# Performance work log

Measured on AMD Instinct MI355X. Metric: run time of the kernel, lower is better.

Reference implementation:

```python
import jax, jax.numpy as jnp
import numpy as np
from jax.ops import segment_sum, segment_max

N = 10000       # nodes
E = 320000      # edges (avg degree 32)
IN_FEATS = 256
HID = 128
HEADS = 4


def setup_inputs() -> dict:
    key = jax.random.key(0)
    ks = jax.random.split(key, 12)
    s = lambda fan_in: 1.0 / np.sqrt(fan_in)
    return {
        "features": jax.random.normal(ks[0], (N, IN_FEATS), jnp.float32),
        "src": jax.random.randint(ks[1], (E,), 0, N, jnp.int32),
        "dst": jax.random.randint(ks[2], (E,), 0, N, jnp.int32),
        # GraphConv 1: in_feats -> hidden
        "W1": jax.random.normal(ks[3], (IN_FEATS, HID), jnp.float32) * s(IN_FEATS),
        "b1": jnp.zeros((HID,), jnp.float32),
        # GraphConv 2: hidden -> hidden
        "W2": jax.random.normal(ks[4], (HID, HID), jnp.float32) * s(HID),
        "b2": jnp.zeros((HID,), jnp.float32),
        # GraphConv 3: hidden -> 1
        "W3": jax.random.normal(ks[5], (HID, 1), jnp.float32) * s(HID),
        "b3": jnp.zeros((1,), jnp.float32),
        # GATConv(hidden, hidden, num_heads=4)
        "Wg": jax.random.normal(ks[6], (HID, HEADS * HID), jnp.float32) * s(HID),
        "attn_l": jax.random.normal(ks[7], (HEADS, HID), jnp.float32) * s(HID),
        "attn_r": jax.random.normal(ks[8], (HEADS, HID), jnp.float32) * s(HID),
        "bg": jnp.zeros((HEADS * HID,), jnp.float32),
    }


def _graph_conv(src, dst, x, W, b):
    """DGL GraphConv with norm='both': D_dst^{-1/2} A D_src^{-1/2} x W + b."""
    ones = jnp.ones((src.shape[0],), x.dtype)
    deg_out = jnp.clip(segment_sum(ones, src, num_segments=N), 1.0)
    deg_in = jnp.clip(segment_sum(ones, dst, num_segments=N), 1.0)
    h = (x * deg_out[:, None] ** -0.5) @ W          # [N, out]
    agg = segment_sum(h[src], dst, num_segments=N)   # gather+scatter over edges
    return agg * deg_in[:, None] ** -0.5 + b


def _gat_conv(src, dst, x, Wg, attn_l, attn_r, bg):
    """DGL GATConv, num_heads=4, negative_slope=0.2. Returns (out, alpha)."""
    z = (x @ Wg).reshape(N, HEADS, HID)             # [N,H,D]
    el = jnp.einsum("nhd,hd->nh", z, attn_l)        # [N,H]
    er = jnp.einsum("nhd,hd->nh", z, attn_r)
    e = jax.nn.leaky_relu(el[src] + er[dst], 0.2)   # [E,H]
    # edge softmax over incoming edges of each dst node
    m = segment_max(e, dst, num_segments=N)          # [N,H]
    ex = jnp.exp(e - m[dst])
    denom = segment_sum(ex, dst, num_segments=N)     # [N,H]
    alpha = ex / denom[dst]                          # [E,H]
    out = segment_sum(alpha[:, :, None] * z[src], dst, num_segments=N)  # [N,H,D]
    return out + bg.reshape(1, HEADS, HID), alpha


def reference(features, src, dst, W1, b1, W2, b2, W3, b3, Wg, attn_l, attn_r, bg):
    h = jax.nn.relu(_graph_conv(src, dst, features, W1, b1))
    h = jax.nn.relu(_graph_conv(src, dst, h, W2, b2))
    h, alpha = _gat_conv(src, dst, h, Wg, attn_l, attn_r, bg)
    h = h.mean(axis=1)                               # mean over heads -> [N,HID]
    risk_scores = jax.nn.sigmoid(_graph_conv(src, dst, h, W3, b3))  # [N,1]
    return risk_scores
```

## Files before the change

kernel.cpp:

```cpp
#include <hip/hip_runtime.h>
#include <hip/hip_bf16.h>

#define NODES   10000
#define EDGES   320000
#define INF_    256
#define HIDF    128
#define NHEADS  4
#define SLOTS   64

#define NB_W1     128
#define NB_ZERO   79
#define PREP_BLKS (NB_W1 + NB_ZERO)

#define FILL_BLKS  1250
#define G1_TILES   157
#define B_W2T      (FILL_BLKS + G1_TILES)
#define NB_W2      64
#define B_FOLD     (B_W2T + NB_W2)
#define B_CDOT     (B_FOLD + 2)
#define FG_BLKS    (B_CDOT + 1)

typedef __attribute__((ext_vector_type(8))) short short8v;
typedef __attribute__((ext_vector_type(4))) float f32x4;

__device__ __forceinline__ float bf_lo(unsigned z) { return __uint_as_float(z << 16); }
__device__ __forceinline__ float bf_hi(unsigned z) { return __uint_as_float(z & 0xffff0000u); }
__device__ __forceinline__ unsigned short bfr(float x) {
    __hip_bfloat16 b = __float2bfloat16(x);
    return *(unsigned short*)&b;
}

__global__ __launch_bounds__(256)
void prep_slim(const float* __restrict__ W1, unsigned short* __restrict__ W1t,
               int* __restrict__ cnt_dego) {
    int b = blockIdx.x, t = threadIdx.x;
    if (b < NB_W1) {
        int id = b * 256 + t;
        int nn = id >> 8, k = id & 255;
        W1t[id] = bfr(W1[k * HIDF + nn]);
        return;
    }
    int id = (b - NB_W1) * 256 + t;
    if (id < 2 * NODES) cnt_dego[id] = 0;
}

__global__ __launch_bounds__(256)
void fill_gemm1(const int* __restrict__ src, const int* __restrict__ dst,
                int* __restrict__ cnt, int* __restrict__ deg_o,
                unsigned short* __restrict__ csr, const float* __restrict__ feat,
                const unsigned short* __restrict__ W1t, unsigned short* __restrict__ Z1,
                const float* __restrict__ W2, unsigned short* __restrict__ W2t,
                const float* __restrict__ Wg, const float* __restrict__ attn_l,
                const float* __restrict__ attn_r, const float* __restrict__ bg,
                const float* __restrict__ W3, float* __restrict__ WL,
                float* __restrict__ WR, float* __restrict__ WV, float* __restrict__ cdot) {
    int b = blockIdx.x, t = threadIdx.x;
    if (b < FILL_BLKS) {
        int e = b * 256 + t;
        int s = src[e], d = dst[e];
        atomicAdd(&deg_o[s], 1);
        int pos = atomicAdd(&cnt[d], 1);
        csr[(d << 6) + pos] = (unsigned short)s;
        return;
    }
    if (b < B_W2T) {
        int vt = b - FILL_BLKS;
        int w = t >> 6, l = t & 63;
        int m0 = vt * 64 + w * 16;
        int lm = l & 15, lk = (l >> 4) * 8;
        int arow = min(m0 + lm, NODES - 1);
        const float4* Af = (const float4*)(feat + (size_t)arow * INF_ + lk);
        const short8v* Bp[8];
#pragma unroll
        for (int cg = 0; cg < 8; ++cg)
            Bp[cg] = (const short8v*)(W1t + (size_t)(cg * 16 + lm) * INF_ + lk);
        f32x4 acc[8];
#pragma unroll
        for (int cg = 0; cg < 8; ++cg) acc[cg] = (f32x4){0.f, 0.f, 0.f, 0.f};
#pragma unroll
        for (int kk = 0; kk < 8; ++kk) {
            float4 f0 = Af[kk * 8];
            float4 f1 = Af[kk * 8 + 1];
            short8v a = {(short)bfr(f0.x), (short)bfr(f0.y), (short)bfr(f0.z), (short)bfr(f0.w),
                         (short)bfr(f1.x), (short)bfr(f1.y), (short)bfr(f1.z), (short)bfr(f1.w)};
#pragma unroll
            for (int cg = 0; cg < 8; ++cg)
                acc[cg] = __builtin_amdgcn_mfma_f32_16x16x32_bf16(a, Bp[cg][kk * 4], acc[cg], 0, 0, 0);
        }
        int rb = m0 + (l >> 4) * 4;
#pragma unroll
        for (int cg = 0; cg < 8; ++cg) {
            int c = cg * 16 + lm;
#pragma unroll
            for (int r = 0; r < 4; ++r) {
                int row = rb + r;
                if (row < NODES) Z1[(size_t)row * HIDF + c] = bfr(acc[cg][r]);
            }
        }
        return;
    }
    if (b < B_FOLD) {
        int id = (b - B_W2T) * 256 + t;
        int nn = id >> 7, k = id & 127;
        W2t[id] = bfr(W2[k * HIDF + nn]);
        return;
    }
    if (b < B_CDOT) {
        int id = (b - B_FOLD) * 256 + t;
        int k = id >> 2, h = id & 3;
        float a = 0.f, bb = 0.f, c = 0.f;
        for (int d = 0; d < HIDF; ++d) {
            float w = Wg[k * 512 + h * HIDF + d];
            a  = fmaf(w, attn_l[h * HIDF + d], a);
            bb = fmaf(w, attn_r[h * HIDF + d], bb);
            c  = fmaf(w, W3[d], c);
        }
        WL[id] = a; WR[id] = bb; WV[id] = c;
        return;
    }
    {
        if (t < 64) {
            float s = 0.f;
            for (int d = t; d < HIDF; d += 64)
                s += (bg[d] + bg[d + 128] + bg[d + 256] + bg[d + 384]) * W3[d];
#pragma unroll
            for (int off = 32; off; off >>= 1) s += __shfl_xor(s, off, 64);
            if (t == 0) cdot[0] = 0.25f * s;
        }
    }
}

__global__ __launch_bounds__(256)
void g1_gemm2(const int* __restrict__ deg_i, const int* __restrict__ deg_o,
              const unsigned short* __restrict__ csr, const unsigned short* __restrict__ Z1,
              const float* __restrict__ b1, const unsigned short* __restrict__ W2t,
              unsigned short* __restrict__ Z2) {
    __shared__ unsigned short Ht[16][136];
    int t = threadIdx.x;
    int w = t >> 6, l = t & 63;
    int m0 = blockIdx.x * 16;
    int quarter = l >> 4, q = l & 15;
    for (int j = 0; j < 4; ++j) {
        int nl = w * 4 + j;
        int n = m0 + nl;
        float a[8] = {0.f, 0.f, 0.f, 0.f, 0.f, 0.f, 0.f, 0.f};
        float sc = 0.f, so = 0.f;
        if (n < NODES) {
            int cnt = deg_i[n];
            int base = n << 6;
            int i = quarter;
            for (; i + 4 < cnt; i += 8) {
                int s0 = csr[base + i], s1 = csr[base + i + 4];
                float so0 = rsqrtf(fmaxf((float)deg_o[s0], 1.f));
                float so1 = rsqrtf(fmaxf((float)deg_o[s1], 1.f));
                uint4 z0 = *(const uint4*)&Z1[s0 * HIDF + 8 * q];
                uint4 z1 = *(const uint4*)&Z1[s1 * HIDF + 8 * q];
                a[0] = fmaf(so0, bf_lo(z0.x), a[0]); a[1] = fmaf(so0, bf_hi(z0.x), a[1]);
                a[2] = fmaf(so0, bf_lo(z0.y), a[2]); a[3] = fmaf(so0, bf_hi(z0.y), a[3]);
                a[4] = fmaf(so0, bf_lo(z0.z), a[4]); a[5] = fmaf(so0, bf_hi(z0.z), a[5]);
                a[6] = fmaf(so0, bf_lo(z0.w), a[6]); a[7] = fmaf(so0, bf_hi(z0.w), a[7]);
                a[0] = fmaf(so1, bf_lo(z1.x), a[0]); a[1] = fmaf(so1, bf_hi(z1.x), a[1]);
                a[2] = fmaf(so1, bf_lo(z1.y), a[2]); a[3] = fmaf(so1, bf_hi(z1.y), a[3]);
                a[4] = fmaf(so1, bf_lo(z1.z), a[4]); a[5] = fmaf(so1, bf_hi(z1.z), a[5]);
                a[6] = fmaf(so1, bf_lo(z1.w), a[6]); a[7] = fmaf(so1, bf_hi(z1.w), a[7]);
            }
            if (i < cnt) {
                int s0 = csr[base + i];
                float so0 = rsqrtf(fmaxf((float)deg_o[s0], 1.f));
                uint4 z0 = *(const uint4*)&Z1[s0 * HIDF + 8 * q];
                a[0] = fmaf(so0, bf_lo(z0.x), a[0]); a[1] = fmaf(so0, bf_hi(z0.x), a[1]);
                a[2] = fmaf(so0, bf_lo(z0.y), a[2]); a[3] = fmaf(so0, bf_hi(z0.y), a[3]);
                a[4] = fmaf(so0, bf_lo(z0.z), a[4]); a[5] = fmaf(so0, bf_hi(z0.z), a[5]);
                a[6] = fmaf(so0, bf_lo(z0.w), a[6]); a[7] = fmaf(so0, bf_hi(z0.w), a[7]);
            }
            sc = rsqrtf(fmaxf((float)cnt, 1.f));
            so = rsqrtf(fmaxf((float)deg_o[n], 1.f));
        }
#pragma unroll
        for (int k = 0; k < 8; ++k) {
            a[k] += __shfl_xor(a[k], 16, 64);
            a[k] += __shfl_xor(a[k], 32, 64);
        }
        if (l < 16) {
            float v[8];
#pragma unroll
            for (int k = 0; k < 8; ++k)
                v[k] = fmaxf(fmaf(a[k], sc, b1[8 * q + k]), 0.f) * so;
            uint4 o;
            o.x = ((unsigned)bfr(v[1]) << 16) | bfr(v[0]);
            o.y = ((unsigned)bfr(v[3]) << 16) | bfr(v[2]);
            o.z = ((unsigned)bfr(v[5]) << 16) | bfr(v[4]);
            o.w = ((unsigned)bfr(v[7]) << 16) | bfr(v[6]);
            *(uint4*)&Ht[nl][8 * q] = o;
        }
    }
    __syncthreads();
    int lm = l & 15, lk = (l >> 4) * 8;
    const unsigned short* arow = &Ht[lm][lk];
    const short8v* Bp0 = (const short8v*)(W2t + (size_t)(w * 16 + lm) * HIDF + lk);
    const short8v* Bp1 = (const short8v*)(W2t + (size_t)((w + 4) * 16 + lm) * HIDF + lk);
    f32x4 acc0 = {0.f, 0.f, 0.f, 0.f}, acc1 = acc0;
#pragma unroll
    for (int kk = 0; kk < 4; ++kk) {
        short8v av = *(const short8v*)(arow + kk * 32);
        acc0 = __builtin_amdgcn_mfma_f32_16x16x32_bf16(av, Bp0[kk * 4], acc0, 0, 0, 0);
        acc1 = __builtin_amdgcn_mfma_f32_16x16x32_bf16(av, Bp1[kk * 4], acc1, 0, 0, 0);
    }
    int rb = m0 + (l >> 4) * 4;
#pragma unroll
    for (int r = 0; r < 4; ++r) {
        int row = rb + r;
        if (row < NODES) {
            Z2[(size_t)row * HIDF + w * 16 + lm]       = bfr(acc0[r]);
            Z2[(size_t)row * HIDF + (w + 4) * 16 + lm] = bfr(acc1[r]);
        }
    }
}

__global__ __launch_bounds__(64)
void gather2(const int* __restrict__ deg_i, const unsigned short* __restrict__ csr,
             const unsigned short* __restrict__ Z2, const float* __restrict__ b2,
             const float* __restrict__ WL, const float* __restrict__ WR,
             const float* __restrict__ WV, float* __restrict__ el,
             float* __restrict__ er, float* __restrict__ zeta) {
    int n = blockIdx.x, l = threadIdx.x;
    int quarter = l >> 4, q = l & 15;
    int cnt = deg_i[n], base = n << 6;
    float a[8] = {0.f, 0.f, 0.f, 0.f, 0.f, 0.f, 0.f, 0.f};
    int i = quarter;
    for (; i + 4 < cnt; i += 8) {
        int s0 = csr[base + i], s1 = csr[base + i + 4];
        uint4 z0 = *(const uint4*)&Z2[s0 * HIDF + 8 * q];
        uint4 z1 = *(const uint4*)&Z2[s1 * HIDF + 8 * q];
        a[0] += bf_lo(z0.x); a[1] += bf_hi(z0.x);
        a[2] += bf_lo(z0.y); a[3] += bf_hi(z0.y);
        a[4] += bf_lo(z0.z); a[5] += bf_hi(z0.z);
        a[6] += bf_lo(z0.w); a[7] += bf_hi(z0.w);
        a[0] += bf_lo(z1.x); a[1] += bf_hi(z1.x);
        a[2] += bf_lo(z1.y); a[3] += bf_hi(z1.y);
        a[4] += bf_lo(z1.z); a[5] += bf_hi(z1.z);
        a[6] += bf_lo(z1.w); a[7] += bf_hi(z1.w);
    }
    if (i < cnt) {
        int s0 = csr[base + i];
        uint4 z0 = *(const uint4*)&Z2[s0 * HIDF + 8 * q];
        a[0] += bf_lo(z0.x); a[1] += bf_hi(z0.x);
        a[2] += bf_lo(z0.y); a[3] += bf_hi(z0.y);
        a[4] += bf_lo(z0.z); a[5] += bf_hi(z0.z);
        a[6] += bf_lo(z0.w); a[7] += bf_hi(z0.w);
    }
#pragma unroll
    for (int k = 0; k < 8; ++k) {
        a[k] += __shfl_xor(a[k], 16, 64);
        a[k] += __shfl_xor(a[k], 32, 64);
    }
    float sc = rsqrtf(fmaxf((float)cnt, 1.f));
    float v[8];
#pragma unroll
    for (int k = 0; k < 8; ++k) v[k] = fmaxf(fmaf(a[k], sc, b2[8 * q + k]), 0.f);
    float elh[NHEADS] = {0.f, 0.f, 0.f, 0.f};
    float erh[NHEADS] = {0.f, 0.f, 0.f, 0.f};
    float zth[NHEADS] = {0.f, 0.f, 0.f, 0.f};
#pragma unroll
    for (int k = 0; k < 8; ++k) {
        int kc = 8 * q + k;
#pragma unroll
        for (int h = 0; h < NHEADS; ++h) {
            elh[h] = fmaf(v[k], WL[kc * NHEADS + h], elh[h]);
            erh[h] = fmaf(v[k], WR[kc * NHEADS + h], erh[h]);
            zth[h] = fmaf(v[k], WV[kc * NHEADS + h], zth[h]);
        }
    }
#pragma unroll
    for (int h = 0; h < NHEADS; ++h) {
#pragma unroll
        for (int off = 1; off <= 8; off <<= 1) {
            elh[h] += __shfl_xor(elh[h], off, 64);
            erh[h] += __shfl_xor(erh[h], off, 64);
            zth[h] += __shfl_xor(zth[h], off, 64);
        }
    }
    if (l == 0) {
#pragma unroll
        for (int h = 0; h < NHEADS; ++h) {
            el[n * NHEADS + h] = elh[h];
            er[n * NHEADS + h] = erh[h];
            zeta[n * NHEADS + h] = zth[h];
        }
    }
}

__global__ __launch_bounds__(64)
void gat_s1(const int* __restrict__ deg_i, const int* __restrict__ deg_o,
            const unsigned short* __restrict__ csr, const float4* __restrict__ el4,
            const float4* __restrict__ er4, const float4* __restrict__ zeta4,
            const float* __restrict__ cdot, float* __restrict__ s1v) {
    int n = blockIdx.x, l = threadIdx.x;
    int cnt = deg_i[n], base = n << 6;
    float4 ern = er4[n];
    float lg[4] = {-1e30f, -1e30f, -1e30f, -1e30f};
    float zt[4] = {0.f, 0.f, 0.f, 0.f};
    bool act = l < cnt;
    if (act) {
        int s = csr[base + l];
        float4 e = el4[s], z = zeta4[s];
        float t;
        t = e.x + ern.x; lg[0] = t > 0.f ? t : 0.2f * t; zt[0] = z.x;
        t = e.y + ern.y; lg[1] = t > 0.f ? t : 0.2f * t; zt[1] = z.y;
        t = e.z + ern.z; lg[2] = t > 0.f ? t : 0.2f * t; zt[2] = z.z;
        t = e.w + ern.w; lg[3] = t > 0.f ? t : 0.2f * t; zt[3] = z.w;
    }
    float m[4], den[4], acc[4];
#pragma unroll
    for (int h = 0; h < 4; ++h) m[h] = lg[h];
#pragma unroll
    for (int off = 32; off; off >>= 1)
#pragma unroll
        for (int h = 0; h < 4; ++h) m[h] = fmaxf(m[h], __shfl_xor(m[h], off, 64));
#pragma unroll
    for (int h = 0; h < 4; ++h) {
        float e0 = act ? __expf(lg[h] - m[h]) : 0.f;
        den[h] = e0;
        acc[h] = e0 * zt[h];
    }
#pragma unroll
    for (int off = 32; off; off >>= 1)
#pragma unroll
        for (int h = 0; h < 4; ++h) {
            den[h] += __shfl_xor(den[h], off, 64);
            acc[h] += __shfl_xor(acc[h], off, 64);
        }
    if (l == 0) {
        float s = 0.f;
#pragma unroll
        for (int h = 0; h < 4; ++h) s += den[h] > 0.f ? acc[h] / den[h] : 0.f;
        float inv_o = rsqrtf(fmaxf((float)deg_o[n], 1.f));
        s1v[n] = inv_o * (0.25f * s + cdot[0]);
    }
}

__global__ __launch_bounds__(64)
void gc3(const int* __restrict__ deg_i, const unsigned short* __restrict__ csr,
         const float* __restrict__ s1v, const float* __restrict__ b3,
         float* __restrict__ out) {
    int n = blockIdx.x, l = threadIdx.x;
    int cnt = deg_i[n], base = n << 6;
    float acc = (l < cnt) ? s1v[csr[base + l]] : 0.f;
#pragma unroll
    for (int off = 32; off; off >>= 1) acc += __shfl_xor(acc, off, 64);
    if (l == 0) {
        float inv_i = rsqrtf(fmaxf((float)cnt, 1.f));
        float xv = acc * inv_i + b3[0];
        out[n] = 1.f / (1.f + __expf(-xv));
    }
}

extern "C" void kernel_launch(void* const* d_in, const int* in_sizes, int n_in,
                              void* d_out, int out_size, void* d_ws, size_t ws_size,
                              hipStream_t stream) {
    const float* feat   = (const float*)d_in[0];
    const int*   src    = (const int*)d_in[1];
    const int*   dst    = (const int*)d_in[2];
    const float* W1     = (const float*)d_in[3];
    const float* b1     = (const float*)d_in[4];
    const float* W2     = (const float*)d_in[5];
    const float* b2     = (const float*)d_in[6];
    const float* W3     = (const float*)d_in[7];
    const float* b3     = (const float*)d_in[8];
    const float* Wg     = (const float*)d_in[9];
    const float* attn_l = (const float*)d_in[10];
    const float* attn_r = (const float*)d_in[11];
    const float* bg     = (const float*)d_in[12];

    char* w = (char*)d_ws;
    auto alloc = [&](size_t bytes) { void* p = (void*)w; w += (bytes + 255) & ~(size_t)255; return p; };
    int*   cnt     = (int*)alloc(2 * NODES * 4);
    int*   deg_o   = cnt + NODES;
    unsigned short* csr = (unsigned short*)alloc((size_t)NODES * SLOTS * 2);
    unsigned short* W1t = (unsigned short*)alloc(128 * 256 * 2);
    unsigned short* W2t = (unsigned short*)alloc(128 * 128 * 2);
    float* WL      = (float*)alloc(HIDF * NHEADS * 4);
    float* WR      = (float*)alloc(HIDF * NHEADS * 4);
    float* WV      = (float*)alloc(HIDF * NHEADS * 4);
    float* cdot    = (float*)alloc(256);
    float* el      = (float*)alloc(NODES * NHEADS * 4);
    float* er      = (float*)alloc(NODES * NHEADS * 4);
    float* zeta    = (float*)alloc(NODES * NHEADS * 4);
    float* s1v     = (float*)alloc(NODES * 4);
    unsigned short* Z1  = (unsigned short*)alloc((size_t)NODES * HIDF * 2);
    unsigned short* Z2  = (unsigned short*)alloc((size_t)NODES * HIDF * 2);

    prep_slim<<<PREP_BLKS, 256, 0, stream>>>(W1, W1t, cnt);
    fill_gemm1<<<FG_BLKS, 256, 0, stream>>>(src, dst, cnt, deg_o, csr, feat, W1t, Z1,
                                            W2, W2t, Wg, attn_l, attn_r, bg, W3,
                                            WL, WR, WV, cdot);
    g1_gemm2<<<(NODES + 15) / 16, 256, 0, stream>>>(cnt, deg_o, csr, Z1, b1, W2t, Z2);
    gather2<<<NODES, 64, 0, stream>>>(cnt, csr, Z2, b2, WL, WR, WV, el, er, zeta);
    gat_s1<<<NODES, 64, 0, stream>>>(cnt, deg_o, csr, (const float4*)el,
                                     (const float4*)er, (const float4*)zeta, cdot, s1v);
    gc3<<<NODES, 64, 0, stream>>>(cnt, csr, s1v, b3, (float*)d_out);
}
```

Measured before the change: 139.4 us.

## Pad degree counters to cache lines, pre-convert features to bf16, split GEMM1 tiles

Degree and in-count arrays are now padded so each node's counter sits on its own 64-byte line, which is meant to reduce atomic contention from false sharing during CSR fill. Features are converted to bf16 in the prep kernel, so the first GEMM reads bf16 directly. Its tiles are halved in N to double the block count, and the GEMM blocks are reordered to launch before the fill blocks. The cost is a 5 MB extra bf16 feature buffer written and reread, and degree reads that are now strided, so each counter read touches its own cache line in the later gather kernels.

```diff
diff --git a/kernel.cpp b/kernel.cpp
--- a/kernel.cpp
+++ b/kernel.cpp
@@ -10,11 +10,14 @@
 
 #define NB_W1     128
 #define NB_ZERO   79
-#define PREP_BLKS (NB_W1 + NB_ZERO)
-
+#define B_FEAT1   (NB_W1 + NB_ZERO)
+#define NB_FEAT   625
+#define PREP_BLKS (B_FEAT1 + NB_FEAT)
+
+#define G1_TILES   314
+#define B_FILL     G1_TILES
 #define FILL_BLKS  1250
-#define G1_TILES   157
-#define B_W2T      (FILL_BLKS + G1_TILES)
+#define B_W2T      (B_FILL + FILL_BLKS)
 #define NB_W2      64
 #define B_FOLD     (B_W2T + NB_W2)
 #define B_CDOT     (B_FOLD + 2)
@@ -31,8 +34,9 @@
 }
 
 __global__ __launch_bounds__(256)
-void prep_slim(const float* __restrict__ W1, unsigned short* __restrict__ W1t,
-               int* __restrict__ cnt_dego) {
+void prep_slim(const float* __restrict__ W1, const float* __restrict__ feat,
+               unsigned short* __restrict__ W1t, int* __restrict__ cnt_pad,
+               int* __restrict__ deg_pad, unsigned short* __restrict__ Abf) {
     int b = blockIdx.x, t = threadIdx.x;
     if (b < NB_W1) {
         int id = b * 256 + t;
@@ -40,63 +44,77 @@
         W1t[id] = bfr(W1[k * HIDF + nn]);
         return;
     }
-    int id = (b - NB_W1) * 256 + t;
-    if (id < 2 * NODES) cnt_dego[id] = 0;
+    if (b < B_FEAT1) {
+        int id = (b - NB_W1) * 256 + t;
+        if (id < NODES) cnt_pad[id << 4] = 0;
+        else if (id < 2 * NODES) deg_pad[(id - NODES) << 4] = 0;
+        return;
+    }
+    {
+        int fb = b - B_FEAT1;
+#pragma unroll
+        for (int k = 0; k < 4; ++k) {
+            int id = fb * 1024 + k * 256 + t;
+            float4 v = ((const float4*)feat)[id];
+            uint2 o;
+            o.x = ((unsigned)bfr(v.y) << 16) | bfr(v.x);
+            o.y = ((unsigned)bfr(v.w) << 16) | bfr(v.z);
+            ((uint2*)Abf)[id] = o;
+        }
+    }
 }
 
 __global__ __launch_bounds__(256)
 void fill_gemm1(const int* __restrict__ src, const int* __restrict__ dst,
-                int* __restrict__ cnt, int* __restrict__ deg_o,
-                unsigned short* __restrict__ csr, const float* __restrict__ feat,
-                const unsigned short* __restrict__ W1t, unsigned short* __restrict__ Z1,
+                int* __restrict__ cnt_pad, int* __restrict__ deg_pad,
+                unsigned short* __restrict__ csr,
+                const unsigned short* __restrict__ A, const unsigned short* __restrict__ W1t,
+                unsigned short* __restrict__ Z1,
                 const float* __restrict__ W2, unsigned short* __restrict__ W2t,
                 const float* __restrict__ Wg, const float* __restrict__ attn_l,
                 const float* __restrict__ attn_r, const float* __restrict__ bg,
                 const float* __restrict__ W3, float* __restrict__ WL,
                 float* __restrict__ WR, float* __restrict__ WV, float* __restrict__ cdot) {
     int b = blockIdx.x, t = threadIdx.x;
-    if (b < FILL_BLKS) {
-        int e = b * 256 + t;
-        int s = src[e], d = dst[e];
-        atomicAdd(&deg_o[s], 1);
-        int pos = atomicAdd(&cnt[d], 1);
-        csr[(d << 6) + pos] = (unsigned short)s;
-        return;
-    }
-    if (b < B_W2T) {
-        int vt = b - FILL_BLKS;
+    if (b < B_FILL) {
+        const int K = INF_;
+        int vt = b;
         int w = t >> 6, l = t & 63;
-        int m0 = vt * 64 + w * 16;
+        int m0 = (vt >> 1) * 64 + w * 16;
+        int n0 = (vt & 1) * 64;
         int lm = l & 15, lk = (l >> 4) * 8;
         int arow = min(m0 + lm, NODES - 1);
-        const float4* Af = (const float4*)(feat + (size_t)arow * INF_ + lk);
-        const short8v* Bp[8];
-#pragma unroll
-        for (int cg = 0; cg < 8; ++cg)
-            Bp[cg] = (const short8v*)(W1t + (size_t)(cg * 16 + lm) * INF_ + lk);
-        f32x4 acc[8];
-#pragma unroll
-        for (int cg = 0; cg < 8; ++cg) acc[cg] = (f32x4){0.f, 0.f, 0.f, 0.f};
-#pragma unroll
-        for (int kk = 0; kk < 8; ++kk) {
-            float4 f0 = Af[kk * 8];
-            float4 f1 = Af[kk * 8 + 1];
-            short8v a = {(short)bfr(f0.x), (short)bfr(f0.y), (short)bfr(f0.z), (short)bfr(f0.w),
-                         (short)bfr(f1.x), (short)bfr(f1.y), (short)bfr(f1.z), (short)bfr(f1.w)};
-#pragma unroll
-            for (int cg = 0; cg < 8; ++cg)
-                acc[cg] = __builtin_amdgcn_mfma_f32_16x16x32_bf16(a, Bp[cg][kk * 4], acc[cg], 0, 0, 0);
+        const short8v* Ap = (const short8v*)(A + (size_t)arow * K + lk);
+        const short8v* Bp = (const short8v*)(W1t + (size_t)(n0 + lm) * K + lk);
+        f32x4 acc0 = {0.f, 0.f, 0.f, 0.f}, acc1 = acc0, acc2 = acc0, acc3 = acc0;
+        const int BS = 2 * K;
+#pragma unroll
+        for (int kk = 0; kk < K / 32; ++kk) {
+            short8v a = Ap[kk * 4];
+            acc0 = __builtin_amdgcn_mfma_f32_16x16x32_bf16(a, Bp[kk * 4], acc0, 0, 0, 0);
+            acc1 = __builtin_amdgcn_mfma_f32_16x16x32_bf16(a, Bp[kk * 4 + BS], acc1, 0, 0, 0);
+            acc2 = __builtin_amdgcn_mfma_f32_16x16x32_bf16(a, Bp[kk * 4 + 2 * BS], acc2, 0, 0, 0);
+            acc3 = __builtin_amdgcn_mfma_f32_16x16x32_bf16(a, Bp[kk * 4 + 3 * BS], acc3, 0, 0, 0);
         }
         int rb = m0 + (l >> 4) * 4;
-#pragma unroll
-        for (int cg = 0; cg < 8; ++cg) {
-            int c = cg * 16 + lm;
+        int cb = n0 + lm;
+        f32x4 accs[4] = {acc0, acc1, acc2, acc3};
+#pragma unroll
+        for (int j = 0; j < 4; ++j) {
 #pragma unroll
             for (int r = 0; r < 4; ++r) {
                 int row = rb + r;
-                if (row < NODES) Z1[(size_t)row * HIDF + c] = bfr(acc[cg][r]);
+                if (row < NODES) Z1[(size_t)row * HIDF + cb + 16 * j] = bfr(accs[j][r]);
             }
         }
+        return;
+    }
+    if (b < B_W2T) {
+        int e = (b - B_FILL) * 256 + t;
+        int s = src[e], d = dst[e];
+        atomicAdd(&deg_pad[s << 4], 1);
+        int pos = atomicAdd(&cnt_pad[d << 4], 1);
+        csr[(d << 6) + pos] = (unsigned short)s;
         return;
     }
     if (b < B_FOLD) {
@@ -131,7 +149,7 @@
 }
 
 __global__ __launch_bounds__(256)
-void g1_gemm2(const int* __restrict__ deg_i, const int* __restrict__ deg_o,
+void g1_gemm2(const int* __restrict__ cnt_pad, const int* __restrict__ deg_pad,
               const unsigned short* __restrict__ csr, const unsigned short* __restrict__ Z1,
               const float* __restrict__ b1, const unsigned short* __restrict__ W2t,
               unsigned short* __restrict__ Z2) {
@@ -146,13 +164,13 @@
         float a[8] = {0.f, 0.f, 0.f, 0.f, 0.f, 0.f, 0.f, 0.f};
         float sc = 0.f, so = 0.f;
         if (n < NODES) {
-            int cnt = deg_i[n];
+            int cnt = cnt_pad[n << 4];
             int base = n << 6;
             int i = quarter;
             for (; i + 4 < cnt; i += 8) {
                 int s0 = csr[base + i], s1 = csr[base + i + 4];
-                float so0 = rsqrtf(fmaxf((float)deg_o[s0], 1.f));
-                float so1 = rsqrtf(fmaxf((float)deg_o[s1], 1.f));
+                float so0 = rsqrtf(fmaxf((float)deg_pad[s0 << 4], 1.f));
+                float so1 = rsqrtf(fmaxf((float)deg_pad[s1 << 4], 1.f));
                 uint4 z0 = *(const uint4*)&Z1[s0 * HIDF + 8 * q];
                 uint4 z1 = *(const uint4*)&Z1[s1 * HIDF + 8 * q];
                 a[0] = fmaf(so0, bf_lo(z0.x), a[0]); a[1] = fmaf(so0, bf_hi(z0.x), a[1]);
@@ -166,7 +184,7 @@
             }
             if (i < cnt) {
                 int s0 = csr[base + i];
-                float so0 = rsqrtf(fmaxf((float)deg_o[s0], 1.f));
+                float so0 = rsqrtf(fmaxf((float)deg_pad[s0 << 4], 1.f));
                 uint4 z0 = *(const uint4*)&Z1[s0 * HIDF + 8 * q];
                 a[0] = fmaf(so0, bf_lo(z0.x), a[0]); a[1] = fmaf(so0, bf_hi(z0.x), a[1]);
                 a[2] = fmaf(so0, bf_lo(z0.y), a[2]); a[3] = fmaf(so0, bf_hi(z0.y), a[3]);
@@ -174,7 +192,7 @@
                 a[6] = fmaf(so0, bf_lo(z0.w), a[6]); a[7] = fmaf(so0, bf_hi(z0.w), a[7]);
             }
             sc = rsqrtf(fmaxf((float)cnt, 1.f));
-            so = rsqrtf(fmaxf((float)deg_o[n], 1.f));
+            so = rsqrtf(fmaxf((float)deg_pad[n << 4], 1.f));
         }
 #pragma unroll
         for (int k = 0; k < 8; ++k) {
@@ -218,14 +236,14 @@
 }
 
 __global__ __launch_bounds__(64)
-void gather2(const int* __restrict__ deg_i, const unsigned short* __restrict__ csr,
+void gather2(const int* __restrict__ cnt_pad, const unsigned short* __restrict__ csr,
              const unsigned short* __restrict__ Z2, const float* __restrict__ b2,
              const float* __restrict__ WL, const float* __restrict__ WR,
              const float* __restrict__ WV, float* __restrict__ el,
              float* __restrict__ er, float* __restrict__ zeta) {
     int n = blockIdx.x, l = threadIdx.x;
     int quarter = l >> 4, q = l & 15;
-    int cnt = deg_i[n], base = n << 6;
+    int cnt = cnt_pad[n << 4], base = n << 6;
     float a[8] = {0.f, 0.f, 0.f, 0.f, 0.f, 0.f, 0.f, 0.f};
     int i = quarter;
     for (; i + 4 < cnt; i += 8) {
@@ -291,12 +309,12 @@
 }
 
 __global__ __launch_bounds__(64)
-void gat_s1(const int* __restrict__ deg_i, const int* __restrict__ deg_o,
+void gat_s1(const int* __restrict__ cnt_pad, const int* __restrict__ deg_pad,
             const unsigned short* __restrict__ csr, const float4* __restrict__ el4,
             const float4* __restrict__ er4, const float4* __restrict__ zeta4,
             const float* __restrict__ cdot, float* __restrict__ s1v) {
     int n = blockIdx.x, l = threadIdx.x;
-    int cnt = deg_i[n], base = n << 6;
+    int cnt = cnt_pad[n << 4], base = n << 6;
     float4 ern = er4[n];
     float lg[4] = {-1e30f, -1e30f, -1e30f, -1e30f};
     float zt[4] = {0.f, 0.f, 0.f, 0.f};
@@ -334,17 +352,17 @@
         float s = 0.f;
 #pragma unroll
         for (int h = 0; h < 4; ++h) s += den[h] > 0.f ? acc[h] / den[h] : 0.f;
-        float inv_o = rsqrtf(fmaxf((float)deg_o[n], 1.f));
+        float inv_o = rsqrtf(fmaxf((float)deg_pad[n << 4], 1.f));
         s1v[n] = inv_o * (0.25f * s + cdot[0]);
     }
 }
 
 __global__ __launch_bounds__(64)
-void gc3(const int* __restrict__ deg_i, const unsigned short* __restrict__ csr,
+void gc3(const int* __restrict__ cnt_pad, const unsigned short* __restrict__ csr,
          const float* __restrict__ s1v, const float* __restrict__ b3,
          float* __restrict__ out) {
     int n = blockIdx.x, l = threadIdx.x;
-    int cnt = deg_i[n], base = n << 6;
+    int cnt = cnt_pad[n << 4], base = n << 6;
     float acc = (l < cnt) ? s1v[csr[base + l]] : 0.f;
 #pragma unroll
     for (int off = 32; off; off >>= 1) acc += __shfl_xor(acc, off, 64);
@@ -374,8 +392,8 @@
 
     char* w = (char*)d_ws;
     auto alloc = [&](size_t bytes) { void* p = (void*)w; w += (bytes + 255) & ~(size_t)255; return p; };
-    int*   cnt     = (int*)alloc(2 * NODES * 4);
-    int*   deg_o   = cnt + NODES;
+    int*   cnt_pad = (int*)alloc((size_t)NODES * 64);
+    int*   deg_pad = (int*)alloc((size_t)NODES * 64);
     unsigned short* csr = (unsigned short*)alloc((size_t)NODES * SLOTS * 2);
     unsigned short* W1t = (unsigned short*)alloc(128 * 256 * 2);
     unsigned short* W2t = (unsigned short*)alloc(128 * 128 * 2);
@@ -387,16 +405,17 @@
     float* er      = (float*)alloc(NODES * NHEADS * 4);
     float* zeta    = (float*)alloc(NODES * NHEADS * 4);
     float* s1v     = (float*)alloc(NODES * 4);
+    unsigned short* Abf = (unsigned short*)alloc((size_t)NODES * INF_ * 2);
     unsigned short* Z1  = (unsigned short*)alloc((size_t)NODES * HIDF * 2);
     unsigned short* Z2  = (unsigned short*)alloc((size_t)NODES * HIDF * 2);
 
-    prep_slim<<<PREP_BLKS, 256, 0, stream>>>(W1, W1t, cnt);
-    fill_gemm1<<<FG_BLKS, 256, 0, stream>>>(src, dst, cnt, deg_o, csr, feat, W1t, Z1,
+    prep_slim<<<PREP_BLKS, 256, 0, stream>>>(W1, feat, W1t, cnt_pad, deg_pad, Abf);
+    fill_gemm1<<<FG_BLKS, 256, 0, stream>>>(src, dst, cnt_pad, deg_pad, csr, Abf, W1t, Z1,
                                             W2, W2t, Wg, attn_l, attn_r, bg, W3,
                                             WL, WR, WV, cdot);
-    g1_gemm2<<<(NODES + 15) / 16, 256, 0, stream>>>(cnt, deg_o, csr, Z1, b1, W2t, Z2);
-    gather2<<<NODES, 64, 0, stream>>>(cnt, csr, Z2, b2, WL, WR, WV, el, er, zeta);
-    gat_s1<<<NODES, 64, 0, stream>>>(cnt, deg_o, csr, (const float4*)el,
+    g1_gemm2<<<(NODES + 15) / 16, 256, 0, stream>>>(cnt_pad, deg_pad, csr, Z1, b1, W2t, Z2);
+    gather2<<<NODES, 64, 0, stream>>>(cnt_pad, csr, Z2, b2, WL, WR, WV, el, er, zeta);
+    gat_s1<<<NODES, 64, 0, stream>>>(cnt_pad, deg_pad, csr, (const float4*)el,
                                      (const float4*)er, (const float4*)zeta, cdot, s1v);
-    gc3<<<NODES, 64, 0, stream>>>(cnt, csr, s1v, b3, (float*)d_out);
-}
+    gc3<<<NODES, 64, 0, stream>>>(cnt_pad, csr, s1v, b3, (float*)d_out);
+}
```

After: 119.3 us, median of 2. 1.17x faster.
